# Optimization experiments

Measured on AMD Instinct MI355X. Metric: run time of the kernel, lower is better.

## Reference

```python
import jax, jax.numpy as jnp
import numpy as np

N, E = 20000, 320000
D_IN, HID, HEADS, OUT = 256, 64, 8, 64
K1 = int(np.ceil(0.75 * N))   # 15000 nodes after pool1
K2 = int(np.ceil(0.75 * K1))  # 11250 nodes after pool2
NEG = -1e30


def setup_inputs():
    key = jax.random.key(0)
    ks = jax.random.split(key, 24)
    s = 0.1
    rn = lambda k, shape: jax.random.normal(k, shape, jnp.float32) * s
    HH = HEADS * HID  # 512
    p = {}
    p["x"] = jax.random.normal(ks[0], (N, D_IN), jnp.float32)
    p["edge_index"] = jax.random.randint(ks[1], (2, E), 0, N, dtype=jnp.int32)
    # gat1: GATv2Conv(D_IN -> HID, heads=HEADS), concat output dim HH
    p["g1_wl"] = rn(ks[2], (D_IN, HH)); p["g1_wr"] = rn(ks[3], (D_IN, HH))
    p["g1_att"] = rn(ks[4], (HEADS, HID)); p["g1_b"] = jnp.zeros((HH,), jnp.float32)
    # pool1 scoring GNN: GATConv(HH -> 1, heads=1) + SelectTopK weight
    p["p1_w"] = rn(ks[5], (HH, 1)); p["p1_asrc"] = rn(ks[6], (1,)); p["p1_adst"] = rn(ks[7], (1,))
    p["p1_b"] = jnp.zeros((1,), jnp.float32); p["p1_sel"] = rn(ks[8], (1,)) + 0.5
    # gat2: GATv2Conv(HH -> HID, heads=1)
    p["g2_wl"] = rn(ks[9], (HH, HID)); p["g2_wr"] = rn(ks[10], (HH, HID))
    p["g2_att"] = rn(ks[11], (1, HID)); p["g2_b"] = jnp.zeros((HID,), jnp.float32)
    # pool2 scoring GNN: GATConv(HID -> 1)
    p["p2_w"] = rn(ks[12], (HID, 1)); p["p2_asrc"] = rn(ks[13], (1,)); p["p2_adst"] = rn(ks[14], (1,))
    p["p2_b"] = jnp.zeros((1,), jnp.float32); p["p2_sel"] = rn(ks[15], (1,)) + 0.5
    # MLP head
    p["l1_w"] = rn(ks[16], (2 * HH, HH)); p["l1_b"] = jnp.zeros((HH,), jnp.float32)
    d2 = OUT * (HEADS // 2); d3 = OUT * (HEADS // 4)
    p["l2_w"] = rn(ks[17], (HH, d2)); p["l2_b"] = jnp.zeros((d2,), jnp.float32)
    p["l3_w"] = rn(ks[18], (d2, d3)); p["l3_b"] = jnp.zeros((d3,), jnp.float32)
    p["l4_w"] = rn(ks[19], (d3, 2)); p["l4_b"] = jnp.zeros((2,), jnp.float32)
    return p


def _seg_softmax(e, dst, valid, n):
    # numerically stable segment softmax over destination nodes; invalid edges -> 0
    e = jnp.where(valid[:, None], e, NEG)
    m = jax.ops.segment_max(e, dst, num_segments=n)
    ex = jnp.exp(e - m[dst])
    ex = jnp.where(valid[:, None], ex, 0.0)
    den = jax.ops.segment_sum(ex, dst, num_segments=n)
    return ex / den[dst]


def gatv2(x, src, dst, valid, wl, wr, att, b):
    # GATv2Conv: score = att . LeakyReLU(Wl x_src + Wr x_dst), segment softmax, concat heads
    n = x.shape[0]
    h, c = att.shape
    xl = (x @ wl).reshape(n, h, c)
    xr = (x @ wr).reshape(n, h, c)
    loop = jnp.arange(n, dtype=src.dtype)  # add_self_loops=True
    s = jnp.concatenate([src, loop]); d = jnp.concatenate([dst, loop])
    v = jnp.concatenate([valid, jnp.ones((n,), bool)])
    m = jax.nn.leaky_relu(xl[s] + xr[d], 0.2)          # [E', H, C]
    e = jnp.einsum("ehc,hc->eh", m, att)               # [E', H]
    a = _seg_softmax(e, d, v, n)
    out = jax.ops.segment_sum(a[..., None] * xl[s], d, num_segments=n)
    return out.reshape(n, h * c) + b


def gat_score(x, src, dst, valid, w, asrc, adst, b):
    # GATConv(in -> 1, heads=1): per-node scalar projection score
    n = x.shape[0]
    xl = x @ w                                          # [n, 1]
    al = (xl * asrc).sum(-1); ar = (xl * adst).sum(-1)  # [n]
    loop = jnp.arange(n, dtype=src.dtype)
    s = jnp.concatenate([src, loop]); d = jnp.concatenate([dst, loop])
    v = jnp.concatenate([valid, jnp.ones((n,), bool)])
    e = jax.nn.leaky_relu(al[s] + ar[d], 0.2)[:, None]
    a = _seg_softmax(e, d, v, n)
    return jax.ops.segment_sum(a * xl[s], d, num_segments=n) + b


def sag_pool(x, src, dst, valid, k, w, asrc, adst, b, sel_w):
    # SAGPooling: GNN score -> tanh -> top-k -> x[perm]*score, edge filtering via mask
    attn = gat_score(x, src, dst, valid, w, asrc, adst, b)           # [n, 1]
    score = jnp.tanh((attn * sel_w).sum(-1) / jnp.linalg.norm(sel_w))  # SelectTopK
    vals, perm = jax.lax.top_k(score, k)
    xp = x[perm] * vals[:, None]
    new_id = jnp.full((x.shape[0],), -1, src.dtype).at[perm].set(jnp.arange(k, dtype=src.dtype))
    s2, d2 = new_id[src], new_id[dst]
    v2 = valid & (s2 >= 0) & (d2 >= 0)
    return xp, jnp.where(v2, s2, 0), jnp.where(v2, d2, 0), v2


def _forward(x, edge_index, g1_wl, g1_wr, g1_att, g1_b, p1_w, p1_asrc, p1_adst, p1_b, p1_sel,
             g2_wl, g2_wr, g2_att, g2_b, p2_w, p2_asrc, p2_adst, p2_b, p2_sel,
             l1_w, l1_b, l2_w, l2_b, l3_w, l3_b, l4_w, l4_b):
    src, dst = edge_index[0], edge_index[1]
    valid = jnp.ones((src.shape[0],), bool)
    h = jax.nn.relu(gatv2(x, src, dst, valid, g1_wl, g1_wr, g1_att, g1_b))
    h, s1, d1, v1 = sag_pool(h, src, dst, valid, K1, p1_w, p1_asrc, p1_adst, p1_b, p1_sel)
    # single graph -> global pools are plain reductions over nodes
    x1 = jnp.concatenate([h.max(0, keepdims=True), h.mean(0, keepdims=True)], axis=1)
    h2 = jax.nn.relu(gatv2(h, s1, d1, v1, g2_wl, g2_wr, g2_att, g2_b))
    h2, _, _, _ = sag_pool(h2, s1, d1, v1, K2, p2_w, p2_asrc, p2_adst, p2_b, p2_sel)
    gmax = jnp.tile(h2.max(0, keepdims=True), (1, HEADS))
    gmean = jnp.tile(h2.mean(0, keepdims=True), (1, HEADS))
    z = x1 + jnp.concatenate([gmax, gmean], axis=1)
    z = jax.nn.relu(z @ l1_w + l1_b)   # dropout is identity at eval
    z = jax.nn.relu(z @ l2_w + l2_b)
    z = jax.nn.relu(z @ l3_w + l3_b)
    logits = z @ l4_w + l4_b
    return logits, jax.nn.softmax(logits, axis=-1)


def reference(x, edge_index, g1_wl, g1_wr, g1_att, g1_b, p1_w, p1_asrc, p1_adst, p1_b, p1_sel,
              g2_wl, g2_wr, g2_att, g2_b, p2_w, p2_asrc, p2_adst, p2_b, p2_sel,
              l1_w, l1_b, l2_w, l2_b, l3_w, l3_b, l4_w, l4_b):
    return _forward(x, edge_index, g1_wl, g1_wr, g1_att, g1_b, p1_w, p1_asrc, p1_adst, p1_b, p1_sel,
                    g2_wl, g2_wr, g2_att, g2_b, p2_w, p2_asrc, p2_adst, p2_b, p2_sel,
                    l1_w, l1_b, l2_w, l2_b, l3_w, l3_b, l4_w, l4_b)
```

## Files before the change

### kernel.cpp

```cpp
#include <hip/hip_runtime.h>
#include <math.h>

#define N_NODES 20000
#define E_EDGES 320000
#define DIN     256
#define HHD     512
#define HIDD    64
#define NHEADS  8
#define K1N     15000
#define K2N     11250

typedef unsigned short u16;
typedef __attribute__((ext_vector_type(8))) short bf16x8;
typedef __attribute__((ext_vector_type(4))) float f32x4;

static inline int cdiv(long long a, long long b) { return (int)((a + b - 1) / b); }

__device__ __forceinline__ void atomicMaxF(float* addr, float val) {
  int* ai = (int*)addr;
  int old = __float_as_int(*addr);
  while (__int_as_float(old) < val) {
    int assumed = old;
    old = atomicCAS(ai, assumed, __float_as_int(val));
    if (old == assumed) break;
  }
}

__device__ __forceinline__ u16 f2bf(float x) {
  unsigned u = __float_as_uint(x);
  return (u16)((u + 0x7FFFu + ((u >> 16) & 1u)) >> 16);
}
__device__ __forceinline__ float bfval(u16 b) { return __uint_as_float(((unsigned)b) << 16); }

__global__ void init_all(int* deg1, int* rank1, float* xls1, float* pools) {
  int i = blockIdx.x * blockDim.x + threadIdx.x;
  if (i < N_NODES) deg1[i] = 0;
  else if (i < 2 * N_NODES) rank1[i - N_NODES] = 0;
  else if (i < 3 * N_NODES) xls1[i - 2 * N_NODES] = 0.f;
  else {
    int idx = i - 3 * N_NODES;
    if (idx < 1152)
      pools[idx] = (idx < 512 || (idx >= 1024 && idx < 1088)) ? -INFINITY : 0.f;
  }
}

__global__ void conv_fused(const float* __restrict__ A, const int* __restrict__ perm,
                           const float* __restrict__ scalev,
                           u16* __restrict__ ah, u16* __restrict__ al, int M, int K,
                           const float* __restrict__ w1, const float* __restrict__ w2,
                           u16* __restrict__ wh, u16* __restrict__ wl, int ncHalf,
                           int aBlocks) {
  if ((int)blockIdx.x < aBlocks) {
    long long i = (long long)blockIdx.x * blockDim.x + threadIdx.x;
    long long e0 = i * 4;
    if (e0 >= (long long)M * K) return;
    int row = (int)(e0 / K), col = (int)(e0 % K);
    int ar = perm ? perm[row] : row;
    float4 v = *(const float4*)(A + (size_t)ar * K + col);
    if (scalev) { float s = scalev[ar]; v.x *= s; v.y *= s; v.z *= s; v.w *= s; }
    u16 h0 = f2bf(v.x), h1 = f2bf(v.y), h2 = f2bf(v.z), h3 = f2bf(v.w);
    u16 l0 = f2bf(v.x - bfval(h0)), l1 = f2bf(v.y - bfval(h1));
    u16 l2 = f2bf(v.z - bfval(h2)), l3 = f2bf(v.w - bfval(h3));
    uint2 hp, lp;
    hp.x = (unsigned)h0 | ((unsigned)h1 << 16); hp.y = (unsigned)h2 | ((unsigned)h3 << 16);
    lp.x = (unsigned)l0 | ((unsigned)l1 << 16); lp.y = (unsigned)l2 | ((unsigned)l3 << 16);
    *(uint2*)(ah + e0) = hp;
    *(uint2*)(al + e0) = lp;
  } else {
    int i = (blockIdx.x - aBlocks) * blockDim.x + threadIdx.x;
    int NT = 2 * ncHalf;
    if (i >= NT * K) return;
    int n = i % NT, k = i / NT;
    float v = (n < ncHalf) ? w1[(size_t)k * ncHalf + n] : w2[(size_t)k * ncHalf + (n - ncHalf)];
    u16 h = f2bf(v);
    u16 l = f2bf(v - bfval(h));
    wh[(size_t)n * K + k] = h;
    wl[(size_t)n * K + k] = l;
  }
}

template<int BT>
__global__ __launch_bounds__(256) void gemm_bf16x3(const u16* __restrict__ ah,
                                                   const u16* __restrict__ al,
                                                   const u16* __restrict__ wh,
                                                   const u16* __restrict__ wl,
                                                   float* __restrict__ c1,
                                                   float* __restrict__ c2,
                                                   int M, int K, int ncHalf) {
  constexpr int F = BT / 32;
  __shared__ u16 Ah[BT][40], Al[BT][40], Bh[BT][40], Bl[BT][40];
  int tid = threadIdx.x;
  int lane = tid & 63, wid = tid >> 6;
  int wr = (wid >> 1) * (BT / 2), wc = (wid & 1) * (BT / 2);
  int brow = blockIdx.y * BT, bcol = blockIdx.x * BT;
  int fr = lane & 15, kg = lane >> 4;
  f32x4 acc[F][F];
#pragma unroll
  for (int i = 0; i < F; i++)
#pragma unroll
    for (int j = 0; j < F; j++) acc[i][j] = (f32x4){0.f, 0.f, 0.f, 0.f};

  for (int k0 = 0; k0 < K; k0 += 32) {
    constexpr int ITER = (BT * 32) / (256 * 8);
#pragma unroll
    for (int i = 0; i < ITER; i++) {
      int pos = tid + i * 256;
      int row = pos >> 2;
      int kc = (pos & 3) * 8;
      int gr = brow + row;
      float4 z = make_float4(0.f, 0.f, 0.f, 0.f);
      float4 vah = (gr < M) ? *(const float4*)(ah + (size_t)gr * K + k0 + kc) : z;
      float4 val = (gr < M) ? *(const float4*)(al + (size_t)gr * K + k0 + kc) : z;
      *(float4*)(&Ah[row][kc]) = vah;
      *(float4*)(&Al[row][kc]) = val;
      int gn = bcol + row;
      *(float4*)(&Bh[row][kc]) = *(const float4*)(wh + (size_t)gn * K + k0 + kc);
      *(float4*)(&Bl[row][kc]) = *(const float4*)(wl + (size_t)gn * K + k0 + kc);
    }
    __syncthreads();
    bf16x8 fa_h[F], fa_l[F], fb_h[F], fb_l[F];
#pragma unroll
    for (int t = 0; t < F; t++) {
      fa_h[t] = *(const bf16x8*)(&Ah[wr + t * 16 + fr][kg * 8]);
      fa_l[t] = *(const bf16x8*)(&Al[wr + t * 16 + fr][kg * 8]);
      fb_h[t] = *(const bf16x8*)(&Bh[wc + t * 16 + fr][kg * 8]);
      fb_l[t] = *(const bf16x8*)(&Bl[wc + t * 16 + fr][kg * 8]);
    }
#pragma unroll
    for (int i = 0; i < F; i++)
#pragma unroll
      for (int j = 0; j < F; j++) {
        acc[i][j] = __builtin_amdgcn_mfma_f32_16x16x32_bf16(fa_h[i], fb_h[j], acc[i][j], 0, 0, 0);
        acc[i][j] = __builtin_amdgcn_mfma_f32_16x16x32_bf16(fa_h[i], fb_l[j], acc[i][j], 0, 0, 0);
        acc[i][j] = __builtin_amdgcn_mfma_f32_16x16x32_bf16(fa_l[i], fb_h[j], acc[i][j], 0, 0, 0);
      }
    __syncthreads();
  }
#pragma unroll
  for (int i = 0; i < F; i++) {
    int r0 = brow + wr + i * 16 + kg * 4;
#pragma unroll
    for (int j = 0; j < F; j++) {
      int cg = bcol + wc + j * 16 + fr;
      float* cp = (cg < ncHalf) ? c1 : c2;
      int cc = (cg < ncHalf) ? cg : cg - ncHalf;
#pragma unroll
      for (int r = 0; r < 4; r++) {
        int gr = r0 + r;
        if (gr < M) cp[(size_t)gr * ncHalf + cc] = acc[i][j][r];
      }
    }
  }
}

__global__ void deg_count(const int* __restrict__ src, const int* __restrict__ dst,
                          const int* __restrict__ newid, int* __restrict__ deg,
                          int nloops) {
  int i = blockIdx.x * blockDim.x + threadIdx.x;
  if (i >= E_EDGES + nloops) return;
  int d;
  if (i < E_EDGES) {
    if (newid) {
      int s = newid[src[i]]; d = newid[dst[i]];
      if (s < 0 || d < 0) return;
    } else d = dst[i];
  } else d = i - E_EDGES;
  atomicAdd(&deg[d], 1);
}

__global__ __launch_bounds__(1024) void scan_excl(const int* deg, int* rowptr,
                                                  int* cursor, int n) {
  __shared__ int wsum[16];
  __shared__ int carry;
  int tid = threadIdx.x, lane = tid & 63, wid = tid >> 6;
  if (tid == 0) { carry = 0; rowptr[0] = 0; }
  __syncthreads();
  for (int base = 0; base < n; base += 1024) {
    int v = (base + tid < n) ? deg[base + tid] : 0;
    int s = v;
#pragma unroll
    for (int off = 1; off < 64; off <<= 1) {
      int t = __shfl_up(s, off);
      if (lane >= off) s += t;
    }
    if (lane == 63) wsum[wid] = s;
    __syncthreads();
    if (wid == 0) {
      int w = (lane < 16) ? wsum[lane] : 0;
#pragma unroll
      for (int off = 1; off < 16; off <<= 1) {
        int t = __shfl_up(w, off);
        if (lane >= off) w += t;
      }
      if (lane < 16) wsum[lane] = w;
    }
    __syncthreads();
    int incl = s + (wid > 0 ? wsum[wid - 1] : 0) + carry;
    if (base + tid < n) { rowptr[base + tid + 1] = incl; cursor[base + tid] = incl - v; }
    __syncthreads();
    if (tid == 1023) carry = incl;
    __syncthreads();
  }
}

__global__ void csr_scatter(const int* __restrict__ src, const int* __restrict__ dst,
                            const int* __restrict__ newid, int* __restrict__ cursor,
                            int* __restrict__ csr_s, int nloops) {
  int i = blockIdx.x * blockDim.x + threadIdx.x;
  if (i >= E_EDGES + nloops) return;
  int s, d;
  if (i < E_EDGES) {
    s = src[i]; d = dst[i];
    if (newid) {
      s = newid[s]; d = newid[d];
      if (s < 0 || d < 0) return;
    }
  } else s = d = i - E_EDGES;
  int pos = atomicAdd(&cursor[d], 1);
  csr_s[pos] = s;
}

__global__ __launch_bounds__(256) void gat1_fused(const int* __restrict__ rowptr,
                                                  const int* __restrict__ csr_s,
                                                  const float* __restrict__ xl,
                                                  const float* __restrict__ xr,
                                                  const float* __restrict__ att,
                                                  const float* __restrict__ bias,
                                                  const float* __restrict__ pw,
                                                  float* __restrict__ out,
                                                  float* __restrict__ xls) {
  int lane = threadIdx.x & 63;
  long long t = (long long)blockIdx.x * blockDim.x + threadIdx.x;
  int gw = (int)(t >> 6);
  int d = gw >> 1;
  if (d >= N_NODES) return;
  int cbase = (gw & 1) * 256 + lane * 4;
  float4 av = *(const float4*)(att + cbase);
  float4 rv = *(const float4*)(xr + (size_t)d * HHD + cbase);
  float m = -INFINITY, den = 0.f;
  float4 acc = make_float4(0.f, 0.f, 0.f, 0.f);
  int b0 = rowptr[d];
  int cnt = rowptr[d + 1] - b0;
  const int* sp = csr_s + b0;

  auto online = [&](float4 v) {
    float p, tv;
    tv = v.x + rv.x; tv = tv > 0.f ? tv : 0.2f * tv; p  = tv * av.x;
    tv = v.y + rv.y; tv = tv > 0.f ? tv : 0.2f * tv; p += tv * av.y;
    tv = v.z + rv.z; tv = tv > 0.f ? tv : 0.2f * tv; p += tv * av.z;
    tv = v.w + rv.w; tv = tv > 0.f ? tv : 0.2f * tv; p += tv * av.w;
    p += __shfl_xor(p, 1); p += __shfl_xor(p, 2); p += __shfl_xor(p, 4); p += __shfl_xor(p, 8);
    float nm = fmaxf(m, p);
    float w  = __expf(p - nm);
    float sc = __expf(m - nm);
    den = den * sc + w;
    acc.x = acc.x * sc + w * v.x;
    acc.y = acc.y * sc + w * v.y;
    acc.z = acc.z * sc + w * v.z;
    acc.w = acc.w * sc + w * v.w;
    m = nm;
  };

  float4 zz = make_float4(0.f, 0.f, 0.f, 0.f);
  float4 A = *(const float4*)(xl + (size_t)sp[0] * HHD + cbase);
  float4 B = (cnt > 1) ? *(const float4*)(xl + (size_t)sp[1] * HHD + cbase) : zz;
  float4 C = (cnt > 2) ? *(const float4*)(xl + (size_t)sp[2] * HHD + cbase) : zz;
  float4 D = (cnt > 3) ? *(const float4*)(xl + (size_t)sp[3] * HHD + cbase) : zz;
  int j = 0;
  for (; j + 4 <= cnt; j += 4) {
    float4 v = A;
    if (j + 4 < cnt) A = *(const float4*)(xl + (size_t)sp[j + 4] * HHD + cbase);
    online(v);
    v = B;
    if (j + 5 < cnt) B = *(const float4*)(xl + (size_t)sp[j + 5] * HHD + cbase);
    online(v);
    v = C;
    if (j + 6 < cnt) C = *(const float4*)(xl + (size_t)sp[j + 6] * HHD + cbase);
    online(v);
    v = D;
    if (j + 7 < cnt) D = *(const float4*)(xl + (size_t)sp[j + 7] * HHD + cbase);
    online(v);
  }
  if (j < cnt) {
    online(A);
    if (j + 1 < cnt) {
      online(B);
      if (j + 2 < cnt) online(C);
    }
  }

  float inv = 1.f / den;
  float4 bv = *(const float4*)(bias + cbase);
  float4 o;
  o.x = acc.x * inv + bv.x; o.y = acc.y * inv + bv.y;
  o.z = acc.z * inv + bv.z; o.w = acc.w * inv + bv.w;
  o.x = o.x > 0.f ? o.x : 0.f; o.y = o.y > 0.f ? o.y : 0.f;
  o.z = o.z > 0.f ? o.z : 0.f; o.w = o.w > 0.f ? o.w : 0.f;
  *(float4*)(out + (size_t)d * HHD + cbase) = o;
  float4 wv = *(const float4*)(pw + cbase);
  float sdot = o.x * wv.x + o.y * wv.y + o.z * wv.z + o.w * wv.w;
#pragma unroll
  for (int off = 32; off > 0; off >>= 1) sdot += __shfl_xor(sdot, off);
  if (lane == 0) atomicAdd(&xls[d], sdot);
}

__global__ __launch_bounds__(256) void gat2_fused(const int* __restrict__ rowptr,
                                                  const int* __restrict__ csr_s,
                                                  const float* __restrict__ xl,
                                                  const float* __restrict__ xr,
                                                  const float* __restrict__ att,
                                                  const float* __restrict__ bias,
                                                  const float* __restrict__ pw,
                                                  float* __restrict__ out,
                                                  float* __restrict__ xls, int n) {
  int lane = threadIdx.x & 63;
  int grp = lane >> 4, li = lane & 15;
  long long t = (long long)blockIdx.x * blockDim.x + threadIdx.x;
  int wv = (int)(t >> 6);
  int d = wv * 4 + grp;
  if (d >= n) return;
  int c0 = li * 4;
  float4 av = *(const float4*)(att + c0);
  float4 rv = *(const float4*)(xr + (size_t)d * HIDD + c0);
  float m = -INFINITY, den = 0.f;
  float4 acc = make_float4(0.f, 0.f, 0.f, 0.f);
  int b0 = rowptr[d];
  int cnt = rowptr[d + 1] - b0;
  const int* sp = csr_s + b0;

  auto online = [&](float4 v) {
    float p, tv;
    tv = v.x + rv.x; tv = tv > 0.f ? tv : 0.2f * tv; p  = tv * av.x;
    tv = v.y + rv.y; tv = tv > 0.f ? tv : 0.2f * tv; p += tv * av.y;
    tv = v.z + rv.z; tv = tv > 0.f ? tv : 0.2f * tv; p += tv * av.z;
    tv = v.w + rv.w; tv = tv > 0.f ? tv : 0.2f * tv; p += tv * av.w;
    p += __shfl_xor(p, 1); p += __shfl_xor(p, 2); p += __shfl_xor(p, 4); p += __shfl_xor(p, 8);
    float nm = fmaxf(m, p);
    float w  = __expf(p - nm);
    float sc = __expf(m - nm);
    den = den * sc + w;
    acc.x = acc.x * sc + w * v.x;
    acc.y = acc.y * sc + w * v.y;
    acc.z = acc.z * sc + w * v.z;
    acc.w = acc.w * sc + w * v.w;
    m = nm;
  };

  float4 zz = make_float4(0.f, 0.f, 0.f, 0.f);
  float4 A = *(const float4*)(xl + (size_t)sp[0] * HIDD + c0);
  float4 B = (cnt > 1) ? *(const float4*)(xl + (size_t)sp[1] * HIDD + c0) : zz;
  int j = 0;
  for (; j + 2 <= cnt; j += 2) {
    float4 v = A;
    if (j + 2 < cnt) A = *(const float4*)(xl + (size_t)sp[j + 2] * HIDD + c0);
    online(v);
    v = B;
    if (j + 3 < cnt) B = *(const float4*)(xl + (size_t)sp[j + 3] * HIDD + c0);
    online(v);
  }
  if (j < cnt) online(A);

  float inv = 1.f / den;
  float4 bv = *(const float4*)(bias + c0);
  float4 o;
  o.x = acc.x * inv + bv.x; o.y = acc.y * inv + bv.y;
  o.z = acc.z * inv + bv.z; o.w = acc.w * inv + bv.w;
  o.x = o.x > 0.f ? o.x : 0.f; o.y = o.y > 0.f ? o.y : 0.f;
  o.z = o.z > 0.f ? o.z : 0.f; o.w = o.w > 0.f ? o.w : 0.f;
  *(float4*)(out + (size_t)d * HIDD + c0) = o;
  float4 wv4 = *(const float4*)(pw + c0);
  float sdot = o.x * wv4.x + o.y * wv4.y + o.z * wv4.z + o.w * wv4.w;
  sdot += __shfl_xor(sdot, 1); sdot += __shfl_xor(sdot, 2);
  sdot += __shfl_xor(sdot, 4); sdot += __shfl_xor(sdot, 8);
  if (li == 0) xls[d] = sdot;
}

__global__ __launch_bounds__(256) void pool_score(const int* __restrict__ rowptr,
                                                  const int* __restrict__ csr_s,
                                                  const float* __restrict__ xls,
                                                  const float* __restrict__ asrc,
                                                  const float* __restrict__ adst,
                                                  const float* __restrict__ bias,
                                                  const float* __restrict__ sel,
                                                  float* __restrict__ score, int n) {
  int d = blockIdx.x * blockDim.x + threadIdx.x;
  if (d >= n) return;
  float as = asrc[0], ad = adst[0];
  float ar = xls[d] * ad;
  int b0 = rowptr[d];
  int cnt = rowptr[d + 1] - b0;
  const int* sp = csr_s + b0;
  float m = -INFINITY, den = 0.f, num = 0.f;
  auto upd = [&](float xs) {
    float e = xs * as + ar;
    e = e > 0.f ? e : 0.2f * e;
    float nm = fmaxf(m, e);
    float scv = __expf(m - nm);
    float ex = __expf(e - nm);
    den = den * scv + ex;
    num = num * scv + ex * xs;
    m = nm;
  };
  float xA = xls[sp[0]];
  float xB = (cnt > 1) ? xls[sp[1]] : 0.f;
  float xC = (cnt > 2) ? xls[sp[2]] : 0.f;
  float xD = (cnt > 3) ? xls[sp[3]] : 0.f;
  int j = 0;
  for (; j + 4 <= cnt; j += 4) {
    float x1 = xA;
    if (j + 4 < cnt) xA = xls[sp[j + 4]];
    upd(x1);
    float x2 = xB;
    if (j + 5 < cnt) xB = xls[sp[j + 5]];
    upd(x2);
    float x3 = xC;
    if (j + 6 < cnt) xC = xls[sp[j + 6]];
    upd(x3);
    float x4 = xD;
    if (j + 7 < cnt) xD = xls[sp[j + 7]];
    upd(x4);
  }
  if (j < cnt) {
    upd(xA);
    if (j + 1 < cnt) {
      upd(xB);
      if (j + 2 < cnt) upd(xC);
    }
  }
  float attn = num / den + bias[0];
  float sv = sel[0];
  score[d] = tanhf(attn * sv / fabsf(sv));
}

#define TK_CHUNK 512
__global__ __launch_bounds__(256) void topk_count(const float* __restrict__ score,
                                                  int* __restrict__ rank, int n,
                                                  int* __restrict__ zbuf, int zn) {
  __shared__ float sc[TK_CHUNK];
  if (zbuf) {
    long long fid = ((long long)blockIdx.y * gridDim.x + blockIdx.x) * 256 + threadIdx.x;
    if (fid < zn) zbuf[fid] = 0;
  }
  int i = blockIdx.x * 256 + threadIdx.x;
  int base = blockIdx.y * TK_CHUNK;
  int cnt = min(TK_CHUNK, n - base);
  for (int j = threadIdx.x; j < cnt; j += 256) sc[j] = score[base + j];
  __syncthreads();
  if (i >= n) return;
  float si = score[i];
  int r = 0;
  for (int j = 0; j < cnt; j++) {
    float sj = sc[j];
    r += (sj > si) || ((sj == si) && ((base + j) < i));
  }
  if (r) atomicAdd(&rank[i], r);
}

__global__ void topk_assign(const int* __restrict__ rank, int* __restrict__ newid,
                            int* __restrict__ perm, int n, int k) {
  int i = blockIdx.x * blockDim.x + threadIdx.x;
  if (i < n) {
    int r = rank[i];
    newid[i] = (r < k) ? r : -1;
    if (r < k) perm[r] = i;
  }
}

__global__ __launch_bounds__(256) void col_pool_conv(const float* __restrict__ X,
                                                     const int* __restrict__ perm,
                                                     const float* __restrict__ scalev,
                                                     float* __restrict__ omax,
                                                     float* __restrict__ osum,
                                                     u16* __restrict__ ah, u16* __restrict__ al,
                                                     const float* __restrict__ w1,
                                                     const float* __restrict__ w2,
                                                     u16* __restrict__ wh, u16* __restrict__ wl,
                                                     int cpBlocks) {
  int tid = threadIdx.x;
  if ((int)blockIdx.x < cpBlocks) {
    float mx[2] = {-INFINITY, -INFINITY};
    float sm[2] = {0.f, 0.f};
    int rpb = (K1N + cpBlocks - 1) / cpBlocks;
    int rbeg = blockIdx.x * rpb;
    int rend = min(K1N, rbeg + rpb);
    for (int r = rbeg; r < rend; r++) {
      int orow = perm[r];
      float sc = scalev[orow];
      const float* row = X + (size_t)orow * HHD;
#pragma unroll
      for (int sg = 0; sg < 2; sg++) {
        int c = sg * 256 + tid;
        float v = row[c] * sc;
        mx[sg] = fmaxf(mx[sg], v);
        sm[sg] += v;
        u16 h = f2bf(v);
        u16 l = f2bf(v - bfval(h));
        ah[(size_t)r * HHD + c] = h;
        al[(size_t)r * HHD + c] = l;
      }
    }
    if (rbeg < rend) {
#pragma unroll
      for (int sg = 0; sg < 2; sg++) {
        int c = sg * 256 + tid;
        atomicMaxF(&omax[c], mx[sg]);
        atomicAdd(&osum[c], sm[sg]);
      }
    }
  } else {
    int i = (blockIdx.x - cpBlocks) * 256 + tid;
    const int NT = 2 * HIDD;
    if (i >= NT * HHD) return;
    int n = i % NT, k = i / NT;
    float v = (n < HIDD) ? w1[(size_t)k * HIDD + n] : w2[(size_t)k * HIDD + (n - HIDD)];
    u16 h = f2bf(v);
    u16 l = f2bf(v - bfval(h));
    wh[(size_t)n * HHD + k] = h;
    wl[(size_t)n * HHD + k] = l;
  }
}

__global__ __launch_bounds__(256) void col_pool(const float* __restrict__ X,
                                                const int* __restrict__ perm,
                                                const float* __restrict__ scalev,
                                                int rows, int C,
                                                float* __restrict__ omax, float* __restrict__ osum) {
  int tid = threadIdx.x;
  float mx = -INFINITY, sm = 0.f;
  int rpb = (rows + gridDim.x - 1) / gridDim.x;
  int rbeg = blockIdx.x * rpb;
  int rend = min(rows, rbeg + rpb);
  for (int r = rbeg; r < rend; r++) {
    int orow = perm[r];
    float sc = scalev[orow];
    int c = tid;
    if (c < C) {
      float v = X[(size_t)orow * C + c] * sc;
      mx = fmaxf(mx, v);
      sm += v;
    }
  }
  if (rbeg < rend && tid < C) {
    atomicMaxF(&omax[tid], mx);
    atomicAdd(&osum[tid], sm);
  }
}

__global__ __launch_bounds__(256) void mlp_l1(const float* __restrict__ pools,
                                              const float* __restrict__ w1,
                                              const float* __restrict__ b1,
                                              float* __restrict__ z1out) {
  __shared__ float z[1024];
  __shared__ float red[16][17];
  int t = threadIdx.x;
  for (int i = t; i < 1024; i += 256) {
    float xv = (i < 512) ? pools[i] : pools[i] * (1.f / K1N);
    float gv = (i < 512) ? pools[1024 + (i & 63)] : pools[1088 + (i & 63)] * (1.f / K2N);
    z[i] = xv + gv;
  }
  __syncthreads();
  int jl = t & 15, ch = t >> 4;
  int j = blockIdx.x * 16 + jl;
  float p = 0.f;
  for (int k = ch * 64; k < ch * 64 + 64; k++) p += z[k] * w1[(size_t)k * 512 + j];
  red[ch][jl] = p;
  __syncthreads();
  if (t < 16) {
    float s = b1[blockIdx.x * 16 + t];
    for (int c = 0; c < 16; c++) s += red[c][t];
    z1out[blockIdx.x * 16 + t] = s > 0.f ? s : 0.f;
  }
}

__global__ __launch_bounds__(256) void mlp_tail(const float* __restrict__ z1,
                                                const float* __restrict__ w2, const float* __restrict__ b2,
                                                const float* __restrict__ w3, const float* __restrict__ b3,
                                                const float* __restrict__ w4, const float* __restrict__ b4,
                                                float* __restrict__ out) {
  __shared__ float z2[256], z3[128], lg[2];
  int t = threadIdx.x;
  {
    float acc = b2[t];
    for (int k = 0; k < 512; k++) acc += z1[k] * w2[(size_t)k * 256 + t];
    z2[t] = acc > 0.f ? acc : 0.f;
  }
  __syncthreads();
  if (t < 128) {
    float acc = b3[t];
    for (int k = 0; k < 256; k++) acc += z2[k] * w3[(size_t)k * 128 + t];
    z3[t] = acc > 0.f ? acc : 0.f;
  }
  __syncthreads();
  if (t < 2) {
    float acc = b4[t];
    for (int k = 0; k < 128; k++) acc += z3[k] * w4[2 * k + t];
    lg[t] = acc;
  }
  __syncthreads();
  if (t == 0) {
    float m = fmaxf(lg[0], lg[1]);
    float e0 = __expf(lg[0] - m), e1 = __expf(lg[1] - m);
    float s = e0 + e1;
    out[0] = lg[0]; out[1] = lg[1];
    out[2] = e0 / s; out[3] = e1 / s;
  }
}

extern "C" void kernel_launch(void* const* d_in, const int* in_sizes, int n_in,
                              void* d_out, int out_size, void* d_ws, size_t ws_size,
                              hipStream_t stream) {
  const float* x       = (const float*)d_in[0];
  const int*   ei      = (const int*)d_in[1];
  const float* g1_wl   = (const float*)d_in[2];
  const float* g1_wr   = (const float*)d_in[3];
  const float* g1_att  = (const float*)d_in[4];
  const float* g1_b    = (const float*)d_in[5];
  const float* p1_w    = (const float*)d_in[6];
  const float* p1_asrc = (const float*)d_in[7];
  const float* p1_adst = (const float*)d_in[8];
  const float* p1_b    = (const float*)d_in[9];
  const float* p1_sel  = (const float*)d_in[10];
  const float* g2_wl   = (const float*)d_in[11];
  const float* g2_wr   = (const float*)d_in[12];
  const float* g2_att  = (const float*)d_in[13];
  const float* g2_b    = (const float*)d_in[14];
  const float* p2_w    = (const float*)d_in[15];
  const float* p2_asrc = (const float*)d_in[16];
  const float* p2_adst = (const float*)d_in[17];
  const float* p2_b    = (const float*)d_in[18];
  const float* p2_sel  = (const float*)d_in[19];
  const float* l1_w    = (const float*)d_in[20];
  const float* l1_b    = (const float*)d_in[21];
  const float* l2_w    = (const float*)d_in[22];
  const float* l2_b    = (const float*)d_in[23];
  const float* l3_w    = (const float*)d_in[24];
  const float* l3_b    = (const float*)d_in[25];
  const float* l4_w    = (const float*)d_in[26];
  const float* l4_b    = (const float*)d_in[27];

  const int* src = ei;
  const int* dst = ei + E_EDGES;

  if (ws_size < (size_t)33440000 * 4) return;
  float* ws  = (float*)d_ws;
  float* xl1 = ws;
  float* xr1 = ws + 10240000;
  float* h1  = ws + 20480000;
  float* aux = ws + 30720000;

  int*   csr_s1   = (int*)aux;
  int*   rowptr1  = (int*)(aux + 340000);
  int*   deg1     = (int*)(aux + 360064);
  int*   rank1    = (int*)(aux + 380064);
  int*   newid1   = (int*)(aux + 400064);
  float* xls1     = aux + 420064;
  float* scr1     = aux + 440064;
  float* pools    = aux + 460064;
  float* x1max    = pools;
  float* x1sum    = pools + 512;
  float* g2max    = pools + 1024;
  float* g2sum    = pools + 1088;
  int*   perm1    = (int*)(aux + 461248);
  float* z1       = aux + 481248;

  u16* ah1 = (u16*)h1;
  u16* al1 = ah1 + 5120000;
  u16* wh1 = al1 + 5120000;
  u16* wl1 = wh1 + 262144;

  u16* ah2 = (u16*)xl1;
  u16* al2 = ah2 + 7680000;
  u16* wh2 = al2 + 7680000;
  u16* wl2 = wh2 + 65536;

  float* a2 = xr1;
  float* xl2      = a2;
  float* xr2      = a2 + 960000;
  float* h2       = a2 + 1920000;
  int*   csr_s2   = (int*)(a2 + 2880000);
  int*   rowptr2  = (int*)(a2 + 3215000);
  int*   deg2     = (int*)(a2 + 3230016);
  int*   rank2    = (int*)(a2 + 3245016);
  int*   newid2   = (int*)(a2 + 3260016);
  float* xls2     = a2 + 3275016;
  float* scr2     = a2 + 3290016;
  int*   perm2    = (int*)(a2 + 3305016);

  dim3 b256(256);
  const int E1 = E_EDGES + N_NODES;
  const int E2 = E_EDGES + K1N;

  init_all<<<cdiv(3 * N_NODES + 1152, 256), b256, 0, stream>>>(deg1, rank1, xls1, pools);
  deg_count<<<cdiv(E1, 256), b256, 0, stream>>>(src, dst, nullptr, deg1, N_NODES);
  scan_excl<<<1, 1024, 0, stream>>>(deg1, rowptr1, deg1, N_NODES);
  csr_scatter<<<cdiv(E1, 256), b256, 0, stream>>>(src, dst, nullptr, deg1, csr_s1, N_NODES);

  {
    int aBlocks = cdiv((long long)N_NODES * DIN / 4, 256);
    int wBlocks = cdiv(2 * HHD * DIN, 256);
    conv_fused<<<aBlocks + wBlocks, b256, 0, stream>>>(
        x, nullptr, nullptr, ah1, al1, N_NODES, DIN, g1_wl, g1_wr, wh1, wl1, HHD, aBlocks);
  }
  gemm_bf16x3<128><<<dim3(2 * HHD / 128, cdiv(N_NODES, 128)), b256, 0, stream>>>(
      ah1, al1, wh1, wl1, xl1, xr1, N_NODES, DIN, HHD);
  gat1_fused<<<cdiv((long long)N_NODES * 128, 256), b256, 0, stream>>>(
      rowptr1, csr_s1, xl1, xr1, g1_att, g1_b, p1_w, h1, xls1);

  pool_score<<<cdiv(N_NODES, 256), b256, 0, stream>>>(rowptr1, csr_s1, xls1,
                                                      p1_asrc, p1_adst, p1_b, p1_sel, scr1, N_NODES);
  topk_count<<<dim3(cdiv(N_NODES, 256), cdiv(N_NODES, TK_CHUNK)), b256, 0, stream>>>(
      scr1, rank1, N_NODES, deg2, 30000);
  topk_assign<<<cdiv(N_NODES, 256), b256, 0, stream>>>(rank1, newid1, perm1, N_NODES, K1N);
  {
    int cpBlocks = 256;
    int wBlocks = cdiv(2 * HIDD * HHD, 256);
    col_pool_conv<<<cpBlocks + wBlocks, b256, 0, stream>>>(
        h1, perm1, scr1, x1max, x1sum, ah2, al2, g2_wl, g2_wr, wh2, wl2, cpBlocks);
  }

  deg_count<<<cdiv(E2, 256), b256, 0, stream>>>(src, dst, newid1, deg2, K1N);
  scan_excl<<<1, 1024, 0, stream>>>(deg2, rowptr2, deg2, K1N);
  csr_scatter<<<cdiv(E2, 256), b256, 0, stream>>>(src, dst, newid1, deg2, csr_s2, K1N);

  gemm_bf16x3<64><<<dim3(2 * HIDD / 64, cdiv(K1N, 64)), b256, 0, stream>>>(
      ah2, al2, wh2, wl2, xl2, xr2, K1N, HHD, HIDD);
  gat2_fused<<<cdiv((long long)K1N * 16, 256), b256, 0, stream>>>(
      rowptr2, csr_s2, xl2, xr2, g2_att, g2_b, p2_w, h2, xls2, K1N);

  pool_score<<<cdiv(K1N, 256), b256, 0, stream>>>(rowptr2, csr_s2, xls2,
                                                  p2_asrc, p2_adst, p2_b, p2_sel, scr2, K1N);
  topk_count<<<dim3(cdiv(K1N, 256), cdiv(K1N, TK_CHUNK)), b256, 0, stream>>>(
      scr2, rank2, K1N, nullptr, 0);
  topk_assign<<<cdiv(K1N, 256), b256, 0, stream>>>(rank2, newid2, perm2, K1N, K2N);
  col_pool<<<128, b256, 0, stream>>>(h2, perm2, scr2, K2N, HIDD, g2max, g2sum);

  mlp_l1<<<32, b256, 0, stream>>>(pools, l1_w, l1_b, z1);
  mlp_tail<<<1, b256, 0, stream>>>(z1, l2_w, l2_b, l3_w, l3_b, l4_w, l4_b, (float*)d_out);
}
```

Baseline: 553.6 us.

## Store GAT1 projections in bf16, one wave per node, 4 scores per thread in top-k

The first GEMM now writes xl/xr as bf16 instead of fp32. This halves the bytes gathered per edge in gat1_fused, which now uses one 64-lane wave per node with 8 channels per lane, and the per-node score is written directly instead of atomically accumulated, so its zero-init is dropped. topk_count now has each thread rank 4 scores against the shared chunk, reducing grid size and the number of LDS reads. Rounding the attention inputs to bf16 adds precision loss that could affect top-k selection near ties.

After: 557.9 us. About the same (+0.8%).

```diff
diff --git a/kernel.cpp b/kernel.cpp
--- a/kernel.cpp
+++ b/kernel.cpp
@@ -32,13 +32,19 @@
 }
 __device__ __forceinline__ float bfval(u16 b) { return __uint_as_float(((unsigned)b) << 16); }
 
-__global__ void init_all(int* deg1, int* rank1, float* xls1, float* pools) {
+__device__ __forceinline__ void unpk8(uint4 u, float* v) {
+  v[0] = __uint_as_float(u.x << 16); v[1] = __uint_as_float(u.x & 0xffff0000u);
+  v[2] = __uint_as_float(u.y << 16); v[3] = __uint_as_float(u.y & 0xffff0000u);
+  v[4] = __uint_as_float(u.z << 16); v[5] = __uint_as_float(u.z & 0xffff0000u);
+  v[6] = __uint_as_float(u.w << 16); v[7] = __uint_as_float(u.w & 0xffff0000u);
+}
+
+__global__ void init_all(int* deg1, int* rank1, float* pools) {
   int i = blockIdx.x * blockDim.x + threadIdx.x;
   if (i < N_NODES) deg1[i] = 0;
   else if (i < 2 * N_NODES) rank1[i - N_NODES] = 0;
-  else if (i < 3 * N_NODES) xls1[i - 2 * N_NODES] = 0.f;
   else {
-    int idx = i - 3 * N_NODES;
+    int idx = i - 2 * N_NODES;
     if (idx < 1152)
       pools[idx] = (idx < 512 || (idx >= 1024 && idx < 1088)) ? -INFINITY : 0.f;
   }
@@ -79,13 +85,13 @@
   }
 }
 
-template<int BT>
+template<int BT, bool OUTBF>
 __global__ __launch_bounds__(256) void gemm_bf16x3(const u16* __restrict__ ah,
                                                    const u16* __restrict__ al,
                                                    const u16* __restrict__ wh,
                                                    const u16* __restrict__ wl,
-                                                   float* __restrict__ c1,
-                                                   float* __restrict__ c2,
+                                                   void* __restrict__ c1v,
+                                                   void* __restrict__ c2v,
                                                    int M, int K, int ncHalf) {
   constexpr int F = BT / 32;
   __shared__ u16 Ah[BT][40], Al[BT][40], Bh[BT][40], Bl[BT][40];
@@ -142,12 +148,20 @@
 #pragma unroll
     for (int j = 0; j < F; j++) {
       int cg = bcol + wc + j * 16 + fr;
-      float* cp = (cg < ncHalf) ? c1 : c2;
-      int cc = (cg < ncHalf) ? cg : cg - ncHalf;
+      bool first = (cg < ncHalf);
+      int cc = first ? cg : cg - ncHalf;
 #pragma unroll
       for (int r = 0; r < 4; r++) {
         int gr = r0 + r;
-        if (gr < M) cp[(size_t)gr * ncHalf + cc] = acc[i][j][r];
+        if (gr < M) {
+          if (OUTBF) {
+            u16* cp = first ? (u16*)c1v : (u16*)c2v;
+            cp[(size_t)gr * ncHalf + cc] = f2bf(acc[i][j][r]);
+          } else {
+            float* cp = first ? (float*)c1v : (float*)c2v;
+            cp[(size_t)gr * ncHalf + cc] = acc[i][j][r];
+          }
+        }
       }
     }
   }
@@ -222,8 +236,8 @@
 
 __global__ __launch_bounds__(256) void gat1_fused(const int* __restrict__ rowptr,
                                                   const int* __restrict__ csr_s,
-                                                  const float* __restrict__ xl,
-                                                  const float* __restrict__ xr,
+                                                  const u16* __restrict__ xlb,
+                                                  const u16* __restrict__ xrb,
                                                   const float* __restrict__ att,
                                                   const float* __restrict__ bias,
                                                   const float* __restrict__ pw,
@@ -231,55 +245,60 @@
                                                   float* __restrict__ xls) {
   int lane = threadIdx.x & 63;
   long long t = (long long)blockIdx.x * blockDim.x + threadIdx.x;
-  int gw = (int)(t >> 6);
-  int d = gw >> 1;
+  int d = (int)(t >> 6);
   if (d >= N_NODES) return;
-  int cbase = (gw & 1) * 256 + lane * 4;
-  float4 av = *(const float4*)(att + cbase);
-  float4 rv = *(const float4*)(xr + (size_t)d * HHD + cbase);
+  int base = lane * 8;
+  float4 a0 = *(const float4*)(att + base);
+  float4 a1 = *(const float4*)(att + base + 4);
+  float r[8];
+  unpk8(*(const uint4*)(xrb + (size_t)d * HHD + base), r);
   float m = -INFINITY, den = 0.f;
-  float4 acc = make_float4(0.f, 0.f, 0.f, 0.f);
+  float acc[8] = {0.f, 0.f, 0.f, 0.f, 0.f, 0.f, 0.f, 0.f};
   int b0 = rowptr[d];
   int cnt = rowptr[d + 1] - b0;
   const int* sp = csr_s + b0;
 
-  auto online = [&](float4 v) {
+  auto online = [&](uint4 u) {
+    float v[8];
+    unpk8(u, v);
     float p, tv;
-    tv = v.x + rv.x; tv = tv > 0.f ? tv : 0.2f * tv; p  = tv * av.x;
-    tv = v.y + rv.y; tv = tv > 0.f ? tv : 0.2f * tv; p += tv * av.y;
-    tv = v.z + rv.z; tv = tv > 0.f ? tv : 0.2f * tv; p += tv * av.z;
-    tv = v.w + rv.w; tv = tv > 0.f ? tv : 0.2f * tv; p += tv * av.w;
-    p += __shfl_xor(p, 1); p += __shfl_xor(p, 2); p += __shfl_xor(p, 4); p += __shfl_xor(p, 8);
+    tv = v[0] + r[0]; tv = tv > 0.f ? tv : 0.2f * tv; p  = tv * a0.x;
+    tv = v[1] + r[1]; tv = tv > 0.f ? tv : 0.2f * tv; p += tv * a0.y;
+    tv = v[2] + r[2]; tv = tv > 0.f ? tv : 0.2f * tv; p += tv * a0.z;
+    tv = v[3] + r[3]; tv = tv > 0.f ? tv : 0.2f * tv; p += tv * a0.w;
+    tv = v[4] + r[4]; tv = tv > 0.f ? tv : 0.2f * tv; p += tv * a1.x;
+    tv = v[5] + r[5]; tv = tv > 0.f ? tv : 0.2f * tv; p += tv * a1.y;
+    tv = v[6] + r[6]; tv = tv > 0.f ? tv : 0.2f * tv; p += tv * a1.z;
+    tv = v[7] + r[7]; tv = tv > 0.f ? tv : 0.2f * tv; p += tv * a1.w;
+    p += __shfl_xor(p, 1); p += __shfl_xor(p, 2); p += __shfl_xor(p, 4);
     float nm = fmaxf(m, p);
     float w  = __expf(p - nm);
     float sc = __expf(m - nm);
     den = den * sc + w;
-    acc.x = acc.x * sc + w * v.x;
-    acc.y = acc.y * sc + w * v.y;
-    acc.z = acc.z * sc + w * v.z;
-    acc.w = acc.w * sc + w * v.w;
+#pragma unroll
+    for (int k = 0; k < 8; k++) acc[k] = acc[k] * sc + w * v[k];
     m = nm;
   };
 
-  float4 zz = make_float4(0.f, 0.f, 0.f, 0.f);
-  float4 A = *(const float4*)(xl + (size_t)sp[0] * HHD + cbase);
-  float4 B = (cnt > 1) ? *(const float4*)(xl + (size_t)sp[1] * HHD + cbase) : zz;
-  float4 C = (cnt > 2) ? *(const float4*)(xl + (size_t)sp[2] * HHD + cbase) : zz;
-  float4 D = (cnt > 3) ? *(const float4*)(xl + (size_t)sp[3] * HHD + cbase) : zz;
+  uint4 zz = make_uint4(0u, 0u, 0u, 0u);
+  uint4 A = *(const uint4*)(xlb + (size_t)sp[0] * HHD + base);
+  uint4 B = (cnt > 1) ? *(const uint4*)(xlb + (size_t)sp[1] * HHD + base) : zz;
+  uint4 C = (cnt > 2) ? *(const uint4*)(xlb + (size_t)sp[2] * HHD + base) : zz;
+  uint4 D = (cnt > 3) ? *(const uint4*)(xlb + (size_t)sp[3] * HHD + base) : zz;
   int j = 0;
   for (; j + 4 <= cnt; j += 4) {
-    float4 v = A;
-    if (j + 4 < cnt) A = *(const float4*)(xl + (size_t)sp[j + 4] * HHD + cbase);
-    online(v);
-    v = B;
-    if (j + 5 < cnt) B = *(const float4*)(xl + (size_t)sp[j + 5] * HHD + cbase);
-    online(v);
-    v = C;
-    if (j + 6 < cnt) C = *(const float4*)(xl + (size_t)sp[j + 6] * HHD + cbase);
-    online(v);
-    v = D;
-    if (j + 7 < cnt) D = *(const float4*)(xl + (size_t)sp[j + 7] * HHD + cbase);
-    online(v);
+    uint4 u = A;
+    if (j + 4 < cnt) A = *(const uint4*)(xlb + (size_t)sp[j + 4] * HHD + base);
+    online(u);
+    u = B;
+    if (j + 5 < cnt) B = *(const uint4*)(xlb + (size_t)sp[j + 5] * HHD + base);
+    online(u);
+    u = C;
+    if (j + 6 < cnt) C = *(const uint4*)(xlb + (size_t)sp[j + 6] * HHD + base);
+    online(u);
+    u = D;
+    if (j + 7 < cnt) D = *(const uint4*)(xlb + (size_t)sp[j + 7] * HHD + base);
+    online(u);
   }
   if (j < cnt) {
     online(A);
@@ -290,18 +309,25 @@
   }
 
   float inv = 1.f / den;
-  float4 bv = *(const float4*)(bias + cbase);
-  float4 o;
-  o.x = acc.x * inv + bv.x; o.y = acc.y * inv + bv.y;
-  o.z = acc.z * inv + bv.z; o.w = acc.w * inv + bv.w;
-  o.x = o.x > 0.f ? o.x : 0.f; o.y = o.y > 0.f ? o.y : 0.f;
-  o.z = o.z > 0.f ? o.z : 0.f; o.w = o.w > 0.f ? o.w : 0.f;
-  *(float4*)(out + (size_t)d * HHD + cbase) = o;
-  float4 wv = *(const float4*)(pw + cbase);
-  float sdot = o.x * wv.x + o.y * wv.y + o.z * wv.z + o.w * wv.w;
+  float4 b0v = *(const float4*)(bias + base);
+  float4 b1v = *(const float4*)(bias + base + 4);
+  float o[8];
+  o[0] = acc[0] * inv + b0v.x; o[1] = acc[1] * inv + b0v.y;
+  o[2] = acc[2] * inv + b0v.z; o[3] = acc[3] * inv + b0v.w;
+  o[4] = acc[4] * inv + b1v.x; o[5] = acc[5] * inv + b1v.y;
+  o[6] = acc[6] * inv + b1v.z; o[7] = acc[7] * inv + b1v.w;
+#pragma unroll
+  for (int k = 0; k < 8; k++) o[k] = o[k] > 0.f ? o[k] : 0.f;
+  float* op = out + (size_t)d * HHD + base;
+  *(float4*)(op)     = make_float4(o[0], o[1], o[2], o[3]);
+  *(float4*)(op + 4) = make_float4(o[4], o[5], o[6], o[7]);
+  float4 w0 = *(const float4*)(pw + base);
+  float4 w1 = *(const float4*)(pw + base + 4);
+  float sdot = o[0]*w0.x + o[1]*w0.y + o[2]*w0.z + o[3]*w0.w
+             + o[4]*w1.x + o[5]*w1.y + o[6]*w1.z + o[7]*w1.w;
 #pragma unroll
   for (int off = 32; off > 0; off >>= 1) sdot += __shfl_xor(sdot, off);
-  if (lane == 0) atomicAdd(&xls[d], sdot);
+  if (lane == 0) xls[d] = sdot;
 }
 
 __global__ __launch_bounds__(256) void gat2_fused(const int* __restrict__ rowptr,
@@ -441,19 +467,30 @@
     long long fid = ((long long)blockIdx.y * gridDim.x + blockIdx.x) * 256 + threadIdx.x;
     if (fid < zn) zbuf[fid] = 0;
   }
-  int i = blockIdx.x * 256 + threadIdx.x;
+  int i0 = (blockIdx.x * 256 + threadIdx.x) * 4;
   int base = blockIdx.y * TK_CHUNK;
   int cnt = min(TK_CHUNK, n - base);
   for (int j = threadIdx.x; j < cnt; j += 256) sc[j] = score[base + j];
   __syncthreads();
-  if (i >= n) return;
-  float si = score[i];
-  int r = 0;
+  if (i0 >= n) return;
+  int nv = min(4, n - i0);
+  float s0 = score[i0];
+  float s1 = (nv > 1) ? score[i0 + 1] : 0.f;
+  float s2 = (nv > 2) ? score[i0 + 2] : 0.f;
+  float s3 = (nv > 3) ? score[i0 + 3] : 0.f;
+  int r0 = 0, r1 = 0, r2 = 0, r3 = 0;
   for (int j = 0; j < cnt; j++) {
     float sj = sc[j];
-    r += (sj > si) || ((sj == si) && ((base + j) < i));
-  }
-  if (r) atomicAdd(&rank[i], r);
+    int gj = base + j;
+    r0 += (sj > s0) || ((sj == s0) && (gj < i0));
+    r1 += (sj > s1) || ((sj == s1) && (gj < i0 + 1));
+    r2 += (sj > s2) || ((sj == s2) && (gj < i0 + 2));
+    r3 += (sj > s3) || ((sj == s3) && (gj < i0 + 3));
+  }
+  if (r0) atomicAdd(&rank[i0], r0);
+  if (nv > 1 && r1) atomicAdd(&rank[i0 + 1], r1);
+  if (nv > 2 && r2) atomicAdd(&rank[i0 + 2], r2);
+  if (nv > 3 && r3) atomicAdd(&rank[i0 + 3], r3);
 }
 
 __global__ void topk_assign(const int* __restrict__ rank, int* __restrict__ newid,
@@ -663,6 +700,9 @@
   int*   perm1    = (int*)(aux + 461248);
   float* z1       = aux + 481248;
 
+  u16* xl1b = (u16*)xl1;
+  u16* xr1b = (u16*)xr1;
+
   u16* ah1 = (u16*)h1;
   u16* al1 = ah1 + 5120000;
   u16* wh1 = al1 + 5120000;
@@ -690,7 +730,7 @@
   const int E1 = E_EDGES + N_NODES;
   const int E2 = E_EDGES + K1N;
 
-  init_all<<<cdiv(3 * N_NODES + 1152, 256), b256, 0, stream>>>(deg1, rank1, xls1, pools);
+  init_all<<<cdiv(2 * N_NODES + 1152, 256), b256, 0, stream>>>(deg1, rank1, pools);
   deg_count<<<cdiv(E1, 256), b256, 0, stream>>>(src, dst, nullptr, deg1, N_NODES);
   scan_excl<<<1, 1024, 0, stream>>>(deg1, rowptr1, deg1, N_NODES);
   csr_scatter<<<cdiv(E1, 256), b256, 0, stream>>>(src, dst, nullptr, deg1, csr_s1, N_NODES);
@@ -701,14 +741,14 @@
     conv_fused<<<aBlocks + wBlocks, b256, 0, stream>>>(
         x, nullptr, nullptr, ah1, al1, N_NODES, DIN, g1_wl, g1_wr, wh1, wl1, HHD, aBlocks);
   }
-  gemm_bf16x3<128><<<dim3(2 * HHD / 128, cdiv(N_NODES, 128)), b256, 0, stream>>>(
-      ah1, al1, wh1, wl1, xl1, xr1, N_NODES, DIN, HHD);
-  gat1_fused<<<cdiv((long long)N_NODES * 128, 256), b256, 0, stream>>>(
-      rowptr1, csr_s1, xl1, xr1, g1_att, g1_b, p1_w, h1, xls1);
+  gemm_bf16x3<128, true><<<dim3(2 * HHD / 128, cdiv(N_NODES, 128)), b256, 0, stream>>>(
+      ah1, al1, wh1, wl1, xl1b, xr1b, N_NODES, DIN, HHD);
+  gat1_fused<<<cdiv((long long)N_NODES * 64, 256), b256, 0, stream>>>(
+      rowptr1, csr_s1, xl1b, xr1b, g1_att, g1_b, p1_w, h1, xls1);
 
   pool_score<<<cdiv(N_NODES, 256), b256, 0, stream>>>(rowptr1, csr_s1, xls1,
                                                       p1_asrc, p1_adst, p1_b, p1_sel, scr1, N_NODES);
-  topk_count<<<dim3(cdiv(N_NODES, 256), cdiv(N_NODES, TK_CHUNK)), b256, 0, stream>>>(
+  topk_count<<<dim3(cdiv(N_NODES, 1024), cdiv(N_NODES, TK_CHUNK)), b256, 0, stream>>>(
       scr1, rank1, N_NODES, deg2, 30000);
   topk_assign<<<cdiv(N_NODES, 256), b256, 0, stream>>>(rank1, newid1, perm1, N_NODES, K1N);
   {
@@ -722,14 +762,14 @@
   scan_excl<<<1, 1024, 0, stream>>>(deg2, rowptr2, deg2, K1N);
   csr_scatter<<<cdiv(E2, 256), b256, 0, stream>>>(src, dst, newid1, deg2, csr_s2, K1N);
 
-  gemm_bf16x3<64><<<dim3(2 * HIDD / 64, cdiv(K1N, 64)), b256, 0, stream>>>(
+  gemm_bf16x3<64, false><<<dim3(2 * HIDD / 64, cdiv(K1N, 64)), b256, 0, stream>>>(
       ah2, al2, wh2, wl2, xl2, xr2, K1N, HHD, HIDD);
   gat2_fused<<<cdiv((long long)K1N * 16, 256), b256, 0, stream>>>(
       rowptr2, csr_s2, xl2, xr2, g2_att, g2_b, p2_w, h2, xls2, K1N);
 
   pool_score<<<cdiv(K1N, 256), b256, 0, stream>>>(rowptr2, csr_s2, xls2,
                                                   p2_asrc, p2_adst, p2_b, p2_sel, scr2, K1N);
-  topk_count<<<dim3(cdiv(K1N, 256), cdiv(K1N, TK_CHUNK)), b256, 0, stream>>>(
+  topk_count<<<dim3(cdiv(K1N, 1024), cdiv(K1N, TK_CHUNK)), b256, 0, stream>>>(
       scr2, rank2, K1N, nullptr, 0);
   topk_assign<<<cdiv(K1N, 256), b256, 0, stream>>>(rank2, newid2, perm2, K1N, K2N);
   col_pool<<<128, b256, 0, stream>>>(h2, perm2, scr2, K2N, HIDD, g2max, g2sum);
```
